# Kernel optimization log

Measured on AMD Instinct MI355X. Metric: run time of the kernel, lower is better.

The kernel has to match this reference:

```python
import jax, jax.numpy as jnp
import numpy as np

B, TE, TD, HE, HD = 8, 256, 128, 512, 512


def setup_inputs() -> dict:
    key = jax.random.key(0)
    k1, k2, k3, k4, k5 = jax.random.split(key, 5)
    # scale weights down (original uses 'uniform' init) to keep tanh unsaturated
    return {
        "encoder_out_seq": jax.random.normal(k1, (B, TE, HE), dtype=jnp.float32),
        "decoder_out_seq": jax.random.normal(k2, (B, TD, HD), dtype=jnp.float32),
        "W_a": jax.random.normal(k3, (HE, HE), dtype=jnp.float32) * 0.05,
        "U_a": jax.random.normal(k4, (HD, HE), dtype=jnp.float32) * 0.05,
        "V_a": jax.random.normal(k5, (HE, 1), dtype=jnp.float32) * 0.05,
    }


def reference(encoder_out_seq, decoder_out_seq, W_a, U_a, V_a):
    # Bahdanau additive attention, vectorized over all decoder timesteps
    # (the original loops over Td via K.rnn; steps are independent).
    Ws = jnp.einsum('bte,eh->bth', encoder_out_seq, W_a)   # [B, Te, He]
    Uh = jnp.einsum('bdk,kh->bdh', decoder_out_seq, U_a)   # [B, Td, He]
    # tanh(S.Wa + h.Ua): broadcast to [B, Td, Te, He], contract with V_a
    act = jnp.tanh(Ws[:, None, :, :] + Uh[:, :, None, :])  # [B, Td, Te, He]
    e = jnp.einsum('bdth,ho->bdt', act, V_a)                # [B, Td, Te]
    e = jax.nn.softmax(e, axis=-1)                          # attention weights
    c = jnp.einsum('bdt,bth->bdh', e, encoder_out_seq)      # [B, Td, He] contexts
    return (c, e)
```

## Files before the change

### kernel.cpp

```cpp
#include <hip/hip_runtime.h>

#define B_  8
#define TE_ 256
#define TD_ 128
#define HE_ 512

typedef __attribute__((ext_vector_type(8))) short short8v;
typedef __attribute__((ext_vector_type(4))) float f32x4;
typedef __attribute__((ext_vector_type(2))) float f32x2;

#define C2 2.8853900817779268f

__device__ __forceinline__ float wave_red_add(float s) {
#define DPPADD(CTRL) \
  s += __int_as_float(__builtin_amdgcn_update_dpp(0, __float_as_int(s), CTRL, 0xf, 0xf, true))
  DPPADD(0x111);
  DPPADD(0x112);
  DPPADD(0x114);
  DPPADD(0x118);
  DPPADD(0x142);
  DPPADD(0x143);
#undef DPPADD
  return s;
}

__device__ __forceinline__ float row_red_add(float s) {
#define DPPADD(CTRL) \
  s += __int_as_float(__builtin_amdgcn_update_dpp(0, __float_as_int(s), CTRL, 0xf, 0xf, true))
  DPPADD(0x111);
  DPPADD(0x112);
  DPPADD(0x114);
  DPPADD(0x118);
#undef DPPADD
  return s;
}

__device__ __forceinline__ f32x2 pk_fma(f32x2 a, f32x2 b, f32x2 c) {
  f32x2 d;
  asm("v_pk_fma_f32 %0, %1, %2, %3" : "=v"(d) : "v"(a), "v"(b), "v"(c));
  return d;
}

__global__ __launch_bounds__(512) void gemm_fused(
    const float* __restrict__ enc, const float* __restrict__ dec,
    const float* __restrict__ Wa, const float* __restrict__ Ua,
    float* __restrict__ C) {
  __shared__ short BT[2][32][512];
  const int bid = blockIdx.x;
  const int mt = bid % 24, nt = bid / 24;
  const int m0 = mt * 128, n0 = nt * 32;
  const bool isenc = (mt < 16);
  const float* Bsrc = isenc ? Wa : Ua;
  const float* Asrc = isenc ? enc + (size_t)m0 * 512
                            : dec + (size_t)(m0 - 2048) * 512;
  const int tid = threadIdx.x;
  {
    const int kp = tid >> 3;
    const int c4 = (tid & 7) * 4;
    for (int p = 0; p < 4; ++p) {
      const int k = 2 * kp + p * 128;
      float4 v0 = *(const float4*)(Bsrc + (size_t)k * 512 + n0 + c4);
      float4 v1 = *(const float4*)(Bsrc + (size_t)(k + 1) * 512 + n0 + c4);
      const float a0[4] = {v0.x, v0.y, v0.z, v0.w};
      const float a1[4] = {v1.x, v1.y, v1.z, v1.w};
      const int kc = k >> 3, klo = k & 7;
#pragma unroll
      for (int q = 0; q < 4; ++q) {
        const int n = c4 + q;
        unsigned u0 = __float_as_uint(a0[q]);
        unsigned u1 = __float_as_uint(a1[q]);
        unsigned hi32 = __builtin_amdgcn_perm(u1, u0, 0x07060302);
        float l0 = a0[q] - __uint_as_float(u0 & 0xffff0000u);
        float l1 = a1[q] - __uint_as_float(u1 & 0xffff0000u);
        unsigned lo32 = __builtin_amdgcn_perm(__float_as_uint(l1), __float_as_uint(l0), 0x07060302);
        const int slot = (kc & ~7) | ((kc ^ n) & 7);
        *(unsigned*)&BT[0][n][slot * 8 + klo] = hi32;
        *(unsigned*)&BT[1][n][slot * 8 + klo] = lo32;
      }
    }
  }
  __syncthreads();
  const int w = tid >> 6, lane = tid & 63;
  const int fm = lane & 15, fc = lane >> 4;
  const float* Ap = Asrc + (size_t)(w * 16 + fm) * 512 + fc * 8;
  f32x4 acc0 = {}, acc1 = {};
  float4 pfa[2], pfb[2];
  pfa[0] = *(const float4*)(Ap);
  pfb[0] = *(const float4*)(Ap + 4);
  pfa[1] = *(const float4*)(Ap + 32);
  pfb[1] = *(const float4*)(Ap + 36);
  for (int it = 0; it < 16; ++it) {
    const float4 fa = pfa[it & 1];
    const float4 fb = pfb[it & 1];
    if (it < 14) {
      pfa[it & 1] = *(const float4*)(Ap + (it + 2) * 32);
      pfb[it & 1] = *(const float4*)(Ap + (it + 2) * 32 + 4);
    }
    const float af[8] = {fa.x, fa.y, fa.z, fa.w, fb.x, fb.y, fb.z, fb.w};
    union { unsigned u[4]; short8v s; } ahu, alu;
#pragma unroll
    for (int e = 0; e < 4; ++e) {
      unsigned u0 = __float_as_uint(af[2 * e]);
      unsigned u1 = __float_as_uint(af[2 * e + 1]);
      ahu.u[e] = __builtin_amdgcn_perm(u1, u0, 0x07060302);
      float l0 = af[2 * e]     - __uint_as_float(u0 & 0xffff0000u);
      float l1 = af[2 * e + 1] - __uint_as_float(u1 & 0xffff0000u);
      alu.u[e] = __builtin_amdgcn_perm(__float_as_uint(l1), __float_as_uint(l0), 0x07060302);
    }
    const short8v ah = ahu.s, al = alu.s;
    const int kc = it * 4 + fc;
    const int base = kc & ~7;
    const int s0 = (base | ((kc ^ fm) & 7)) * 8;
    const int s1 = (base | ((kc ^ (16 + fm)) & 7)) * 8;
    short8v bh0 = *(const short8v*)&BT[0][fm][s0];
    short8v bl0 = *(const short8v*)&BT[1][fm][s0];
    short8v bh1 = *(const short8v*)&BT[0][16 + fm][s1];
    short8v bl1 = *(const short8v*)&BT[1][16 + fm][s1];
    acc0 = __builtin_amdgcn_mfma_f32_16x16x32_bf16(ah, bh0, acc0, 0, 0, 0);
    acc1 = __builtin_amdgcn_mfma_f32_16x16x32_bf16(ah, bh1, acc1, 0, 0, 0);
    acc0 = __builtin_amdgcn_mfma_f32_16x16x32_bf16(ah, bl0, acc0, 0, 0, 0);
    acc1 = __builtin_amdgcn_mfma_f32_16x16x32_bf16(ah, bl1, acc1, 0, 0, 0);
    acc0 = __builtin_amdgcn_mfma_f32_16x16x32_bf16(al, bh0, acc0, 0, 0, 0);
    acc1 = __builtin_amdgcn_mfma_f32_16x16x32_bf16(al, bh1, acc1, 0, 0, 0);
  }
  const int row = m0 + w * 16 + fc * 4;
  float* Cp = C + (size_t)row * 512 + n0 + fm;
#pragma unroll
  for (int r = 0; r < 4; ++r)
    Cp[(size_t)r * 512] = __builtin_amdgcn_exp2f(C2 * acc0[r]);
#pragma unroll
  for (int r = 0; r < 4; ++r)
    Cp[(size_t)r * 512 + 16] = __builtin_amdgcn_exp2f(C2 * acc1[r]);
}

__global__ __launch_bounds__(1024) void attn_fused(
    const float* __restrict__ EWs, const float* __restrict__ EU,
    const float* __restrict__ Va, float* __restrict__ e_out) {
  __shared__ float sEU[4][HE_];
  __shared__ float sV[HE_];
  __shared__ float sE4[4][TE_][4];
  __shared__ float sRed[16];
  __shared__ float sNorm[4];
  const int tid = threadIdx.x;
  const int b  = blockIdx.x & 7;
  const int d0 = (blockIdx.x >> 3) * 4;
  if (tid < 512)
    ((float4*)sEU)[tid] = ((const float4*)(EU + (size_t)(b * TD_ + d0) * HE_))[tid];
  else if (tid < 640)
    ((float4*)sV)[tid - 512] = ((const float4*)Va)[tid - 512];
  __syncthreads();
  const int lane = tid & 63, w = tid >> 6;
  const int tb = w * 16;
  const int h0 = lane * 8;
  f32x2 peU[4][4];
  float nvv[8], sumv = 0.f;
#pragma unroll
  for (int j = 0; j < 8; ++j) {
    const float vj = sV[h0 + j];
    sumv += vj;
    nvv[j] = -2.0f * vj;
  }
#pragma unroll
  for (int d = 0; d < 4; ++d)
#pragma unroll
    for (int jj = 0; jj < 4; ++jj)
      peU[d][jj] = ((const f32x2*)&sEU[d][h0])[jj];
  const f32x2 one2 = {1.0f, 1.0f};
  const float* pw = EWs + ((size_t)b * TE_ + tb) * HE_ + h0;
  f32x2 pX[4];
#pragma unroll
  for (int jj = 0; jj < 4; ++jj) pX[jj] = ((const f32x2*)pw)[jj];
  for (int ti = 0; ti < 16; ++ti) {
    const float* pn = pw + HE_;
    f32x2 nX[4];
#pragma unroll
    for (int jj = 0; jj < 4; ++jj) nX[jj] = ((const f32x2*)pn)[jj];
    float s0 = sumv, s1 = sumv, s2 = sumv, s3 = sumv;
#pragma unroll
    for (int jj = 0; jj < 4; ++jj) {
      const float nva = nvv[2 * jj], nvb = nvv[2 * jj + 1];
#define TPAIR(D, SD) { \
      f32x2 ee = pk_fma(pX[jj], peU[D][jj], one2); \
      float num = nva * ee.y; \
      num = fmaf(nvb, ee.x, num); \
      SD = fmaf(num, __builtin_amdgcn_rcpf(ee.x * ee.y), SD); }
      TPAIR(0, s0)
      TPAIR(1, s1)
      TPAIR(2, s2)
      TPAIR(3, s3)
#undef TPAIR
    }
    s0 = row_red_add(s0);
    s1 = row_red_add(s1);
    s2 = row_red_add(s2);
    s3 = row_red_add(s3);
    if ((lane & 15) == 15) {
      const int r = lane >> 4;
      sE4[0][tb + ti][r] = s0;
      sE4[1][tb + ti][r] = s1;
      sE4[2][tb + ti][r] = s2;
      sE4[3][tb + ti][r] = s3;
    }
    pX[0] = nX[0]; pX[1] = nX[1]; pX[2] = nX[2]; pX[3] = nX[3];
    pw = pn;
  }
  __syncthreads();
  const int dA = tid >> 8, t = tid & 255;
  const float* q = sE4[dA][t];
  const float ex = __expf(q[0] + q[1] + q[2] + q[3]);
  float sum = wave_red_add(ex);
  if (lane == 63) sRed[w] = sum;
  __syncthreads();
  if (tid < 4)
    sNorm[tid] = 1.0f / (sRed[tid * 4] + sRed[tid * 4 + 1] + sRed[tid * 4 + 2] + sRed[tid * 4 + 3]);
  __syncthreads();
  e_out[(size_t)(b * TD_ + d0 + dA) * TE_ + t] = ex * sNorm[dA];
}

__global__ __launch_bounds__(512) void ctx_gemm(
    const float* __restrict__ e, const float* __restrict__ enc,
    float* __restrict__ c_out) {
  __shared__ short BT[2][32][256];
  const int bid = blockIdx.x;
  const int b = bid & 7, nt = bid >> 3;
  const int n0 = nt * 32;
  const float* A    = e   + (size_t)b * TD_ * TE_;
  const float* Bsrc = enc + (size_t)b * TE_ * HE_;
  const int tid = threadIdx.x;
  {
    const int kp = tid >> 3;
    const int c4 = (tid & 7) * 4;
    for (int p = 0; p < 2; ++p) {
      const int k = 2 * kp + p * 128;
      float4 v0 = *(const float4*)(Bsrc + (size_t)k * HE_ + n0 + c4);
      float4 v1 = *(const float4*)(Bsrc + (size_t)(k + 1) * HE_ + n0 + c4);
      const float a0[4] = {v0.x, v0.y, v0.z, v0.w};
      const float a1[4] = {v1.x, v1.y, v1.z, v1.w};
      const int kc = k >> 3, klo = k & 7;
#pragma unroll
      for (int q = 0; q < 4; ++q) {
        const int n = c4 + q;
        unsigned u0 = __float_as_uint(a0[q]);
        unsigned u1 = __float_as_uint(a1[q]);
        unsigned hi32 = __builtin_amdgcn_perm(u1, u0, 0x07060302);
        float l0 = a0[q] - __uint_as_float(u0 & 0xffff0000u);
        float l1 = a1[q] - __uint_as_float(u1 & 0xffff0000u);
        unsigned lo32 = __builtin_amdgcn_perm(__float_as_uint(l1), __float_as_uint(l0), 0x07060302);
        const int slot = (kc & ~7) | ((kc ^ n) & 7);
        *(unsigned*)&BT[0][n][slot * 8 + klo] = hi32;
        *(unsigned*)&BT[1][n][slot * 8 + klo] = lo32;
      }
    }
  }
  __syncthreads();
  const int w = tid >> 6, lane = tid & 63;
  const int fm = lane & 15, fc = lane >> 4;
  const float* Ap = A + (size_t)(w * 16 + fm) * TE_ + fc * 8;
  f32x4 acc0 = {}, acc1 = {};
  for (int it = 0; it < 8; ++it) {
    const float4 fa = *(const float4*)(Ap + it * 32);
    const float4 fb = *(const float4*)(Ap + it * 32 + 4);
    const float af[8] = {fa.x, fa.y, fa.z, fa.w, fb.x, fb.y, fb.z, fb.w};
    union { unsigned u[4]; short8v s; } ahu, alu;
#pragma unroll
    for (int q = 0; q < 4; ++q) {
      unsigned u0 = __float_as_uint(af[2 * q]);
      unsigned u1 = __float_as_uint(af[2 * q + 1]);
      ahu.u[q] = __builtin_amdgcn_perm(u1, u0, 0x07060302);
      float l0 = af[2 * q]     - __uint_as_float(u0 & 0xffff0000u);
      float l1 = af[2 * q + 1] - __uint_as_float(u1 & 0xffff0000u);
      alu.u[q] = __builtin_amdgcn_perm(__float_as_uint(l1), __float_as_uint(l0), 0x07060302);
    }
    const short8v ah = ahu.s, al = alu.s;
    const int kc = it * 4 + fc;
    const int base = kc & ~7;
    const int s0 = (base | ((kc ^ fm) & 7)) * 8;
    const int s1 = (base | ((kc ^ (16 + fm)) & 7)) * 8;
    short8v bh0 = *(const short8v*)&BT[0][fm][s0];
    short8v bl0 = *(const short8v*)&BT[1][fm][s0];
    short8v bh1 = *(const short8v*)&BT[0][16 + fm][s1];
    short8v bl1 = *(const short8v*)&BT[1][16 + fm][s1];
    acc0 = __builtin_amdgcn_mfma_f32_16x16x32_bf16(ah, bh0, acc0, 0, 0, 0);
    acc1 = __builtin_amdgcn_mfma_f32_16x16x32_bf16(ah, bh1, acc1, 0, 0, 0);
    acc0 = __builtin_amdgcn_mfma_f32_16x16x32_bf16(ah, bl0, acc0, 0, 0, 0);
    acc1 = __builtin_amdgcn_mfma_f32_16x16x32_bf16(ah, bl1, acc1, 0, 0, 0);
    acc0 = __builtin_amdgcn_mfma_f32_16x16x32_bf16(al, bh0, acc0, 0, 0, 0);
    acc1 = __builtin_amdgcn_mfma_f32_16x16x32_bf16(al, bh1, acc1, 0, 0, 0);
  }
  const int row = w * 16 + fc * 4;
  float* Cp = c_out + (size_t)(b * TD_ + row) * HE_ + n0 + fm;
#pragma unroll
  for (int r = 0; r < 4; ++r) Cp[(size_t)r * HE_] = acc0[r];
#pragma unroll
  for (int r = 0; r < 4; ++r) Cp[(size_t)r * HE_ + 16] = acc1[r];
}

extern "C" void kernel_launch(void* const* d_in, const int* in_sizes, int n_in,
                              void* d_out, int out_size, void* d_ws, size_t ws_size,
                              hipStream_t stream) {
  const float* enc = (const float*)d_in[0];
  const float* dec = (const float*)d_in[1];
  const float* Wa  = (const float*)d_in[2];
  const float* Ua  = (const float*)d_in[3];
  const float* Va  = (const float*)d_in[4];
  float* c_out = (float*)d_out;
  float* e_out = c_out + (size_t)B_ * TD_ * HE_;
  float* Cws = (float*)d_ws;
  const float* EWs = Cws;
  const float* EU  = Cws + (size_t)2048 * 512;
  gemm_fused<<<384, 512, 0, stream>>>(enc, dec, Wa, Ua, Cws);
  attn_fused<<<256, 1024, 0, stream>>>(EWs, EU, Va, e_out);
  ctx_gemm<<<128, 512, 0, stream>>>(e_out, enc, c_out);
}
```

Baseline: 108.4 us.

## Precompute bf16 hi/lo attention weights and split ctx_gemm over M for more blocks

```diff
diff --git a/kernel.cpp b/kernel.cpp
--- a/kernel.cpp
+++ b/kernel.cpp
@@ -135,7 +135,8 @@
 
 __global__ __launch_bounds__(1024) void attn_fused(
     const float* __restrict__ EWs, const float* __restrict__ EU,
-    const float* __restrict__ Va, float* __restrict__ e_out) {
+    const float* __restrict__ Va, float* __restrict__ e_out,
+    unsigned short* __restrict__ Eh, unsigned short* __restrict__ El) {
   __shared__ float sEU[4][HE_];
   __shared__ float sV[HE_];
   __shared__ float sE4[4][TE_][4];
@@ -166,21 +167,23 @@
     for (int jj = 0; jj < 4; ++jj)
       peU[d][jj] = ((const f32x2*)&sEU[d][h0])[jj];
   const f32x2 one2 = {1.0f, 1.0f};
+  union F4 { float4 v; f32x2 h[2]; };
   const float* pw = EWs + ((size_t)b * TE_ + tb) * HE_ + h0;
-  f32x2 pX[4];
-#pragma unroll
-  for (int jj = 0; jj < 4; ++jj) pX[jj] = ((const f32x2*)pw)[jj];
+  F4 a0, a1;
+  a0.v = *(const float4*)(pw);
+  a1.v = *(const float4*)(pw + 4);
   for (int ti = 0; ti < 16; ++ti) {
     const float* pn = pw + HE_;
-    f32x2 nX[4];
-#pragma unroll
-    for (int jj = 0; jj < 4; ++jj) nX[jj] = ((const f32x2*)pn)[jj];
+    F4 nA, nB;
+    nA.v = *(const float4*)(pn);
+    nB.v = *(const float4*)(pn + 4);
     float s0 = sumv, s1 = sumv, s2 = sumv, s3 = sumv;
 #pragma unroll
     for (int jj = 0; jj < 4; ++jj) {
+      const f32x2 xx = (jj < 2) ? a0.h[jj] : a1.h[jj - 2];
       const float nva = nvv[2 * jj], nvb = nvv[2 * jj + 1];
 #define TPAIR(D, SD) { \
-      f32x2 ee = pk_fma(pX[jj], peU[D][jj], one2); \
+      f32x2 ee = pk_fma(xx, peU[D][jj], one2); \
       float num = nva * ee.y; \
       num = fmaf(nvb, ee.x, num); \
       SD = fmaf(num, __builtin_amdgcn_rcpf(ee.x * ee.y), SD); }
@@ -201,7 +204,7 @@
       sE4[2][tb + ti][r] = s2;
       sE4[3][tb + ti][r] = s3;
     }
-    pX[0] = nX[0]; pX[1] = nX[1]; pX[2] = nX[2]; pX[3] = nX[3];
+    a0 = nA; a1 = nB;
     pw = pn;
   }
   __syncthreads();
@@ -214,24 +217,31 @@
   if (tid < 4)
     sNorm[tid] = 1.0f / (sRed[tid * 4] + sRed[tid * 4 + 1] + sRed[tid * 4 + 2] + sRed[tid * 4 + 3]);
   __syncthreads();
-  e_out[(size_t)(b * TD_ + d0 + dA) * TE_ + t] = ex * sNorm[dA];
-}
-
-__global__ __launch_bounds__(512) void ctx_gemm(
-    const float* __restrict__ e, const float* __restrict__ enc,
-    float* __restrict__ c_out) {
+  const float wgt = ex * sNorm[dA];
+  const size_t oi = (size_t)(b * TD_ + d0 + dA) * TE_ + t;
+  e_out[oi] = wgt;
+  const unsigned u = __float_as_uint(wgt);
+  const float lo_f = wgt - __uint_as_float(u & 0xffff0000u);
+  Eh[oi] = (unsigned short)(u >> 16);
+  El[oi] = (unsigned short)(__float_as_uint(lo_f) >> 16);
+}
+
+__global__ __launch_bounds__(256) void ctx_gemm(
+    const unsigned short* __restrict__ Eh, const unsigned short* __restrict__ El,
+    const float* __restrict__ enc, float* __restrict__ c_out) {
   __shared__ short BT[2][32][256];
   const int bid = blockIdx.x;
-  const int b = bid & 7, nt = bid >> 3;
+  const int b = bid & 7;
+  const int nt = (bid >> 3) & 15;
+  const int m0 = (bid >> 7) * 64;
   const int n0 = nt * 32;
-  const float* A    = e   + (size_t)b * TD_ * TE_;
   const float* Bsrc = enc + (size_t)b * TE_ * HE_;
   const int tid = threadIdx.x;
   {
     const int kp = tid >> 3;
     const int c4 = (tid & 7) * 4;
-    for (int p = 0; p < 2; ++p) {
-      const int k = 2 * kp + p * 128;
+    for (int p = 0; p < 4; ++p) {
+      const int k = 2 * kp + p * 64;
       float4 v0 = *(const float4*)(Bsrc + (size_t)k * HE_ + n0 + c4);
       float4 v1 = *(const float4*)(Bsrc + (size_t)(k + 1) * HE_ + n0 + c4);
       const float a0[4] = {v0.x, v0.y, v0.z, v0.w};
@@ -255,23 +265,13 @@
   __syncthreads();
   const int w = tid >> 6, lane = tid & 63;
   const int fm = lane & 15, fc = lane >> 4;
-  const float* Ap = A + (size_t)(w * 16 + fm) * TE_ + fc * 8;
+  const size_t arow = (size_t)(b * TD_ + m0 + w * 16 + fm) * TE_ + fc * 8;
+  const unsigned short* Ah = Eh + arow;
+  const unsigned short* Al = El + arow;
   f32x4 acc0 = {}, acc1 = {};
   for (int it = 0; it < 8; ++it) {
-    const float4 fa = *(const float4*)(Ap + it * 32);
-    const float4 fb = *(const float4*)(Ap + it * 32 + 4);
-    const float af[8] = {fa.x, fa.y, fa.z, fa.w, fb.x, fb.y, fb.z, fb.w};
-    union { unsigned u[4]; short8v s; } ahu, alu;
-#pragma unroll
-    for (int q = 0; q < 4; ++q) {
-      unsigned u0 = __float_as_uint(af[2 * q]);
-      unsigned u1 = __float_as_uint(af[2 * q + 1]);
-      ahu.u[q] = __builtin_amdgcn_perm(u1, u0, 0x07060302);
-      float l0 = af[2 * q]     - __uint_as_float(u0 & 0xffff0000u);
-      float l1 = af[2 * q + 1] - __uint_as_float(u1 & 0xffff0000u);
-      alu.u[q] = __builtin_amdgcn_perm(__float_as_uint(l1), __float_as_uint(l0), 0x07060302);
-    }
-    const short8v ah = ahu.s, al = alu.s;
+    const short8v ah = *(const short8v*)(Ah + it * 32);
+    const short8v al = *(const short8v*)(Al + it * 32);
     const int kc = it * 4 + fc;
     const int base = kc & ~7;
     const int s0 = (base | ((kc ^ fm) & 7)) * 8;
@@ -287,7 +287,7 @@
     acc0 = __builtin_amdgcn_mfma_f32_16x16x32_bf16(al, bh0, acc0, 0, 0, 0);
     acc1 = __builtin_amdgcn_mfma_f32_16x16x32_bf16(al, bh1, acc1, 0, 0, 0);
   }
-  const int row = w * 16 + fc * 4;
+  const int row = m0 + w * 16 + fc * 4;
   float* Cp = c_out + (size_t)(b * TD_ + row) * HE_ + n0 + fm;
 #pragma unroll
   for (int r = 0; r < 4; ++r) Cp[(size_t)r * HE_] = acc0[r];
@@ -308,7 +308,9 @@
   float* Cws = (float*)d_ws;
   const float* EWs = Cws;
   const float* EU  = Cws + (size_t)2048 * 512;
+  unsigned short* Eh = (unsigned short*)((char*)d_ws + (size_t)3072 * 512 * 4);
+  unsigned short* El = Eh + (size_t)B_ * TD_ * TE_;
   gemm_fused<<<384, 512, 0, stream>>>(enc, dec, Wa, Ua, Cws);
-  attn_fused<<<256, 1024, 0, stream>>>(EWs, EU, Va, e_out);
-  ctx_gemm<<<128, 512, 0, stream>>>(e_out, enc, c_out);
-}
+  attn_fused<<<256, 1024, 0, stream>>>(EWs, EU, Va, e_out, Eh, El);
+  ctx_gemm<<<256, 256, 0, stream>>>(Eh, El, enc, c_out);
+}
```

After: 107.0 us. About the same (-1.3%).
